# Kernel tuning notes

Measured on AMD Instinct MI355X. Metric: run time of the kernel, lower is better.

The kernel has to match this reference:

```python
import jax, jax.numpy as jnp
import numpy as np

B, C, H, W = 2, 256, 64, 64
HEADS, DIM_HEAD = 8, 64
INNER = HEADS * DIM_HEAD


def setup_inputs() -> dict:
    key = jax.random.key(0)
    k1, k2, k3, k4 = jax.random.split(key, 4)
    x = jax.random.normal(k1, (B, C, H, W), dtype=jnp.float32)
    # 1x1 conv weights stored as [out_ch, in_ch]
    w_qkv = jax.random.normal(k2, (3 * INNER, C), dtype=jnp.float32) * (1.0 / np.sqrt(C))
    w_out = jax.random.normal(k3, (C, INNER), dtype=jnp.float32) * (1.0 / np.sqrt(INNER))
    b_out = jax.random.normal(k4, (C,), dtype=jnp.float32) * 0.01
    return {"x": x, "w_qkv": w_qkv, "w_out": w_out, "b_out": b_out}


def reference(x, w_qkv, w_out, b_out):
    b, c, h, w = x.shape
    n = h * w
    # 1x1 conv == channel matmul
    qkv = jnp.einsum('oc,bchw->bohw', w_qkv, x)  # [B, 3*inner, H, W]
    qkv = qkv.reshape(b, 3, HEADS, DIM_HEAD, n)
    qkv = jnp.transpose(qkv, (1, 0, 2, 4, 3))    # [3, B, heads, N, dim_head]
    q, k, v = qkv[0], qkv[1], qkv[2]
    scale = 1.0 / (DIM_HEAD ** 0.5)
    dots = jnp.einsum('bhnd,bhmd->bhnm', q, k) * scale  # [B, heads, N, N]
    attn = jax.nn.softmax(dots, axis=-1)
    out = jnp.einsum('bhnm,bhmd->bhnd', attn, v)        # [B, heads, N, dim_head]
    out = jnp.transpose(out, (0, 1, 3, 2)).reshape(b, INNER, h, w)
    return jnp.einsum('ci,bihw->bchw', w_out, out) + b_out[None, :, None, None]
```

## Files before the change

kernel.cpp:

```cpp
#include <hip/hip_runtime.h>
#include <hip/hip_bf16.h>

typedef unsigned short u16;
typedef __attribute__((ext_vector_type(8))) short bf16x8;
typedef __attribute__((ext_vector_type(4))) float f32x4;
typedef __attribute__((ext_vector_type(8))) unsigned short u16x8;
typedef __attribute__((ext_vector_type(4))) unsigned short u16x4;

#define N_POS 4096
#define HEADS 8
#define DHEAD 64
#define CIN   256
#define INNER 512
#define NSPLIT 2
#define JCHUNK (N_POS / NSPLIT)

__device__ __forceinline__ u16 f2bf(float f) {
    union { float f; unsigned int u; } v; v.f = f;
    unsigned int u = v.u + 0x7FFFu + ((v.u >> 16) & 1u);
    return (u16)(u >> 16);
}

__device__ __forceinline__ float bf2f(u16 h) {
    union { float f; unsigned int u; } v; v.u = ((unsigned int)h) << 16;
    return v.f;
}

__device__ __forceinline__ unsigned int pkbf2(float lo, float hi) {
    union { __hip_bfloat162 b; unsigned int u; } cv;
    cv.b = __float22bfloat162_rn(make_float2(lo, hi));
    return cv.u;
}

__global__ __launch_bounds__(256, 2) void k1_qkv(const float* __restrict__ x,
                                                 const float* __restrict__ w_qkv,
                                                 const float* __restrict__ w_out,
                                                 u16* __restrict__ q_ws,
                                                 u16* __restrict__ k_ws,
                                                 u16* __restrict__ vt_ws,
                                                 u16* __restrict__ wo) {
    __shared__ u16 Alds[64 * 40];
    __shared__ u16 Blds[256 * 40];
    int tid = threadIdx.x;
    int by  = blockIdx.y;
    int b   = blockIdx.z;

    if (by == 24) {
        size_t base = ((size_t)((b * 16 + blockIdx.x) * 256 + tid)) * 16;
        const float* src = w_out + base;
        union { unsigned int u[4]; u16x8 v; } o0, o1;
        for (int j = 0; j < 4; ++j) o0.u[j] = pkbf2(src[2 * j],     src[2 * j + 1]);
        for (int j = 0; j < 4; ++j) o1.u[j] = pkbf2(src[8 + 2 * j], src[9 + 2 * j]);
        *(u16x8*)(wo + base)     = o0.v;
        *(u16x8*)(wo + base + 8) = o1.v;
        return;
    }

    int n0  = blockIdx.x * 256;
    int o0  = by * 64;
    int sel = by >> 3;
    int h   = by & 7;
    int wv = tid >> 6, l = tid & 63, quad = l >> 4, l15 = l & 15;
    int srow = tid >> 2, sseg = tid & 3;

    const float* xb = x + (size_t)b * CIN * N_POS + n0 + tid;

    f32x4 acc[16] = {};
    for (int c0 = 0; c0 < CIN; c0 += 32) {
        {
            const float* wqp = w_qkv + (size_t)(o0 + srow) * CIN + c0 + sseg * 8;
            union { unsigned int u[4]; u16x8 v; } av;
            for (int j = 0; j < 4; ++j) av.u[j] = pkbf2(wqp[2 * j], wqp[2 * j + 1]);
            *(u16x8*)&Alds[srow * 40 + sseg * 8] = av.v;
        }
        {
            union { unsigned int u[16]; } tmp;
            #pragma unroll
            for (int j = 0; j < 16; ++j)
                tmp.u[j] = pkbf2(xb[(size_t)(c0 + 2 * j) * N_POS],
                                 xb[(size_t)(c0 + 2 * j + 1) * N_POS]);
            u16* bd = &Blds[tid * 40];
            *(u16x8*)(bd)      = *(u16x8*)&tmp.u[0];
            *(u16x8*)(bd + 8)  = *(u16x8*)&tmp.u[4];
            *(u16x8*)(bd + 16) = *(u16x8*)&tmp.u[8];
            *(u16x8*)(bd + 24) = *(u16x8*)&tmp.u[12];
        }
        __syncthreads();
        bf16x8 af = *(const bf16x8*)&Alds[(wv * 16 + l15) * 40 + quad * 8];
        if (sel < 2) {
            for (int nt = 0; nt < 16; ++nt) {
                bf16x8 bfrag = *(const bf16x8*)&Blds[(nt * 16 + l15) * 40 + quad * 8];
                acc[nt] = __builtin_amdgcn_mfma_f32_16x16x32_bf16(af, bfrag, acc[nt], 0, 0, 0);
            }
        } else {
            for (int nt = 0; nt < 16; ++nt) {
                bf16x8 bfrag = *(const bf16x8*)&Blds[(nt * 16 + l15) * 40 + quad * 8];
                acc[nt] = __builtin_amdgcn_mfma_f32_16x16x32_bf16(bfrag, af, acc[nt], 0, 0, 0);
            }
        }
        __syncthreads();
    }
    const float QSCALE = 0.125f * 1.44269504088896f;
    int bh = b * HEADS + h;
    if (sel < 2) {
        float sc = (sel == 0) ? QSCALE : 1.0f;
        u16* base = (sel == 0) ? q_ws : k_ws;
        int dbase = wv * 16 + quad * 4;
        for (int nt = 0; nt < 16; ++nt) {
            int n = n0 + nt * 16 + l15;
            u16x4 pk;
            for (int r = 0; r < 4; ++r) pk[r] = f2bf(acc[nt][r] * sc);
            *(u16x4*)&base[((size_t)bh * N_POS + n) * DHEAD + dbase] = pk;
        }
    } else {
        int dloc = wv * 16 + l15;
        for (int nt = 0; nt < 16; ++nt) {
            u16x4 pk;
            for (int r = 0; r < 4; ++r) pk[r] = f2bf(acc[nt][r]);
            *(u16x4*)&vt_ws[((size_t)bh * DHEAD + dloc) * N_POS
                            + n0 + nt * 16 + quad * 4] = pk;
        }
    }
}

__global__ __launch_bounds__(256, 2) void k2_attn(const u16* __restrict__ q_ws,
                                                  const u16* __restrict__ k_ws,
                                                  const u16* __restrict__ vt_ws,
                                                  u16* __restrict__ op_ws,
                                                  float* __restrict__ lw_ws) {
    __shared__ u16 Klds[2][64 * 72];
    __shared__ u16 Vlds[2][80 * 72];
    int tid = threadIdx.x;
    int v   = blockIdx.x + (blockIdx.y << 4) + (blockIdx.z << 8);
    int slot = v & 7, idx = v >> 3;
    int bh   = slot * 2 + (idx & 1);
    int q0   = ((idx >> 1) & 15) * 256;
    int half = idx >> 5;
    int jbase = half * JCHUNK;
    int wv = tid >> 6, l = tid & 63, quad = l >> 4, l15 = l & 15;
    int srow = tid >> 2, sseg = tid & 3;
    int srowp = (srow & 0x23) | ((srow & 4) << 2) | ((srow & 0x18) >> 1);
    int kofs = srowp * 72 + sseg * 16;
    int vofs = srow * 72 + sseg * 16;

    const u16* qp = q_ws + ((size_t)(bh * N_POS + q0 + wv * 64 + l15)) * DHEAD + quad * 8;
    bf16x8 bq[4][2];
    for (int it = 0; it < 4; ++it) {
        bq[it][0] = *(const bf16x8*)(qp + (size_t)it * 16 * DHEAD);
        bq[it][1] = *(const bf16x8*)(qp + (size_t)it * 16 * DHEAD + 32);
    }

    f32x4 Oacc[4][5] = {};

    const u16* kp = k_ws + ((size_t)(bh * N_POS + srow)) * DHEAD + sseg * 16;
    const u16* vp = vt_ws + ((size_t)(bh * DHEAD + srow)) * N_POS + sseg * 16;

    {
        int r2 = tid >> 4, c4 = (tid & 15) * 4;
        u16 one = (r2 == 0) ? (u16)0x3F80 : (u16)0;
        u16x4 cv = {one, one, one, one};
        *(u16x4*)&Vlds[0][(64 + r2) * 72 + c4] = cv;
        *(u16x4*)&Vlds[1][(64 + r2) * 72 + c4] = cv;
    }

    u16x8 pf0 = *(const u16x8*)(kp + (size_t)jbase * DHEAD);
    u16x8 pf1 = *(const u16x8*)(kp + (size_t)jbase * DHEAD + 8);
    u16x8 pf2 = *(const u16x8*)(vp + jbase);
    u16x8 pf3 = *(const u16x8*)(vp + jbase + 8);
    *(u16x8*)&Klds[0][kofs]     = pf0;
    *(u16x8*)&Klds[0][kofs + 8] = pf1;
    *(u16x8*)&Vlds[0][vofs]     = pf2;
    *(u16x8*)&Vlds[0][vofs + 8] = pf3;
    {
        const u16* kpj = kp + (size_t)(jbase + 64) * DHEAD;
        pf0 = *(const u16x8*)kpj;
        pf1 = *(const u16x8*)(kpj + 8);
        pf2 = *(const u16x8*)(vp + jbase + 64);
        pf3 = *(const u16x8*)(vp + jbase + 72);
    }
    __syncthreads();

    union PF { unsigned int u[4]; bf16x8 v; };
    int cur = 0;
    for (int j0 = jbase; j0 < jbase + JCHUNK; j0 += 64) {
        if (j0 + 64 < jbase + JCHUNK) {
            *(u16x8*)&Klds[cur ^ 1][kofs]     = pf0;
            *(u16x8*)&Klds[cur ^ 1][kofs + 8] = pf1;
            *(u16x8*)&Vlds[cur ^ 1][vofs]     = pf2;
            *(u16x8*)&Vlds[cur ^ 1][vofs + 8] = pf3;
        }

        PF pfr[4][2];
        f32x4 z0[4], z1[4];

        auto QK = [&](f32x4* z, int p, int a) {
            const u16* kb = &Klds[cur][((2 * p + a) * 16 + l15) * 72 + quad * 8];
            bf16x8 kf0 = *(const bf16x8*)kb;
            bf16x8 kf1 = *(const bf16x8*)(kb + 32);
            __builtin_amdgcn_s_setprio(1);
            #pragma unroll
            for (int it = 0; it < 4; ++it) {
                f32x4 t = {};
                t = __builtin_amdgcn_mfma_f32_16x16x32_bf16(kf0, bq[it][0], t, 0, 0, 0);
                t = __builtin_amdgcn_mfma_f32_16x16x32_bf16(kf1, bq[it][1], t, 0, 0, 0);
                z[it] = t;
            }
            __builtin_amdgcn_s_setprio(0);
        };
        auto EXPPACK = [&](f32x4* z, int p, int a) {
            #pragma unroll
            for (int it = 0; it < 4; ++it) {
                float e0 = __builtin_amdgcn_exp2f(z[it][0]);
                float e1 = __builtin_amdgcn_exp2f(z[it][1]);
                float e2 = __builtin_amdgcn_exp2f(z[it][2]);
                float e3 = __builtin_amdgcn_exp2f(z[it][3]);
                pfr[it][p].u[2 * a]     = pkbf2(e0, e1);
                pfr[it][p].u[2 * a + 1] = pkbf2(e2, e3);
            }
        };
        auto PV = [&](int p, int dt_lo, int dt_hi) {
            __builtin_amdgcn_s_setprio(1);
            for (int dt = dt_lo; dt < dt_hi; ++dt) {
                bf16x8 vf = *(const bf16x8*)&Vlds[cur][(dt * 16 + l15) * 72 + p * 32 + quad * 8];
                #pragma unroll
                for (int it = 0; it < 4; ++it)
                    Oacc[it][dt] = __builtin_amdgcn_mfma_f32_16x16x32_bf16(vf, pfr[it][p].v, Oacc[it][dt], 0, 0, 0);
            }
            __builtin_amdgcn_s_setprio(0);
        };

        QK(z0, 0, 0);
        QK(z1, 0, 1);
        EXPPACK(z0, 0, 0);
        EXPPACK(z1, 0, 1);
        QK(z0, 1, 0);
        PV(0, 0, 2);
        EXPPACK(z0, 1, 0);
        QK(z1, 1, 1);
        PV(0, 2, 5);
        EXPPACK(z1, 1, 1);
        PV(1, 0, 5);

        if (j0 + 128 < jbase + JCHUNK) {
            const u16* kpj = kp + (size_t)(j0 + 128) * DHEAD;
            pf0 = *(const u16x8*)kpj;
            pf1 = *(const u16x8*)(kpj + 8);
            pf2 = *(const u16x8*)(vp + j0 + 128);
            pf3 = *(const u16x8*)(vp + j0 + 136);
        }
        __syncthreads();
        cur ^= 1;
    }

    int b = bh >> 3, h = bh & 7;
    u16* opb = op_ws + (size_t)half * 2 * N_POS * INNER;
    float* lwb = lw_ws + (size_t)half * 2 * HEADS * N_POS;
    for (int it = 0; it < 4; ++it) {
        int n = q0 + wv * 64 + it * 16 + l15;
        if (quad == 0) lwb[(size_t)bh * N_POS + n] = Oacc[it][4][0];
        u16* dst = opb + ((size_t)(b * N_POS + n)) * INNER + h * DHEAD;
        for (int dt = 0; dt < 4; ++dt) {
            u16x4 pk;
            for (int r = 0; r < 4; ++r) pk[r] = f2bf(Oacc[it][dt][r]);
            *(u16x4*)&dst[dt * 16 + quad * 4] = pk;
        }
    }
}

__global__ __launch_bounds__(512) void k3_out(const u16* __restrict__ wo,
                                              const float* __restrict__ b_out,
                                              const u16* __restrict__ op_ws,
                                              const float* __restrict__ lw_ws,
                                              float* __restrict__ out) {
    __shared__ u16 Alds[2][256 * 36];
    __shared__ u16 Blds[16 * 520];
    int tid = threadIdx.x;
    int n0 = blockIdx.x * 16;
    int b  = blockIdx.y;
    int wv = tid >> 6, l = tid & 63, quad = l >> 4, l15 = l & 15;

    {
        int i8 = tid & 63;
        int h  = i8 >> 3;
        for (int p = 0; p < 2; ++p) {
            int nl = p * 8 + (tid >> 6);
            int n = n0 + nl;
            size_t lidx = ((size_t)(b * HEADS + h)) * N_POS + n;
            float ls = lw_ws[lidx] + lw_ws[(size_t)2 * HEADS * N_POS + lidx];
            float inv = 1.0f / ls;
            size_t oidx = ((size_t)(b * N_POS + n)) * INNER + i8 * 8;
            u16x8 pv0 = *(const u16x8*)(op_ws + oidx);
            u16x8 pv1 = *(const u16x8*)(op_ws + (size_t)2 * N_POS * INNER + oidx);
            u16x8 vv;
            for (int k = 0; k < 8; ++k)
                vv[k] = f2bf((bf2f(pv0[k]) + bf2f(pv1[k])) * inv);
            *(u16x8*)&Blds[nl * 520 + i8 * 8] = vv;
        }
    }
    {
        int row = tid >> 1, seg = tid & 1;
        const u16* src = wo + (size_t)row * INNER + seg * 16;
        *(u16x8*)&Alds[0][row * 36 + seg * 16]     = *(const u16x8*)src;
        *(u16x8*)&Alds[0][row * 36 + seg * 16 + 8] = *(const u16x8*)(src + 8);
    }
    __syncthreads();

    f32x4 acc[2] = {};
    int cur = 0;
    for (int s = 0; s < 16; ++s) {
        if (s + 1 < 16) {
            int row = tid >> 1, seg = tid & 1;
            const u16* src = wo + (size_t)row * INNER + (s + 1) * 32 + seg * 16;
            *(u16x8*)&Alds[cur ^ 1][row * 36 + seg * 16]     = *(const u16x8*)src;
            *(u16x8*)&Alds[cur ^ 1][row * 36 + seg * 16 + 8] = *(const u16x8*)(src + 8);
        }
        for (int ac = 0; ac < 2; ++ac) {
            bf16x8 af = *(const bf16x8*)&Alds[cur][(wv * 32 + ac * 16 + l15) * 36 + quad * 8];
            bf16x8 bfrag = *(const bf16x8*)&Blds[l15 * 520 + s * 32 + quad * 8];
            acc[ac] = __builtin_amdgcn_mfma_f32_16x16x32_bf16(af, bfrag, acc[ac], 0, 0, 0);
        }
        __syncthreads();
        cur ^= 1;
    }
    for (int ac = 0; ac < 2; ++ac)
        for (int r = 0; r < 4; ++r) {
            int c = wv * 32 + ac * 16 + quad * 4 + r;
            out[((size_t)(b * CIN + c)) * N_POS + n0 + l15] = acc[ac][r] + b_out[c];
        }
}

extern "C" void kernel_launch(void* const* d_in, const int* in_sizes, int n_in,
                              void* d_out, int out_size, void* d_ws, size_t ws_size,
                              hipStream_t stream) {
    const float* x     = (const float*)d_in[0];
    const float* w_qkv = (const float*)d_in[1];
    const float* w_out = (const float*)d_in[2];
    const float* b_out = (const float*)d_in[3];
    float* out = (float*)d_out;

    u16* ws    = (u16*)d_ws;
    u16* q_ws  = ws;
    u16* k_ws  = q_ws + (size_t)2 * HEADS * N_POS * DHEAD;
    u16* vt_ws = k_ws + (size_t)2 * HEADS * N_POS * DHEAD;
    u16* wo_bf = vt_ws + (size_t)2 * HEADS * N_POS * DHEAD;
    u16* op_ws = wo_bf + (size_t)CIN * INNER;
    float* lw_ws = (float*)(op_ws + (size_t)NSPLIT * 2 * N_POS * INNER);

    hipLaunchKernelGGL(k1_qkv, dim3(16, 25, 2), dim3(256), 0, stream,
                       x, w_qkv, w_out, q_ws, k_ws, vt_ws, wo_bf);
    hipLaunchKernelGGL(k2_attn, dim3(16, 16, NSPLIT), dim3(256), 0, stream,
                       q_ws, k_ws, vt_ws, op_ws, lw_ws);
    hipLaunchKernelGGL(k3_out, dim3(256, 2), dim3(512), 0, stream,
                       wo_bf, b_out, op_ws, lw_ws, out);
}
```

Baseline: 175.1 us.

## Retile QKV projection so each block covers all heads for a 64-position slab

Result: slower. 196.7 us (+12.3%).

```diff
diff --git a/kernel.cpp b/kernel.cpp
--- a/kernel.cpp
+++ b/kernel.cpp
@@ -32,21 +32,22 @@
     return cv.u;
 }
 
-__global__ __launch_bounds__(256, 2) void k1_qkv(const float* __restrict__ x,
+__global__ __launch_bounds__(512, 2) void k1_qkv(const float* __restrict__ x,
                                                  const float* __restrict__ w_qkv,
                                                  const float* __restrict__ w_out,
                                                  u16* __restrict__ q_ws,
                                                  u16* __restrict__ k_ws,
                                                  u16* __restrict__ vt_ws,
                                                  u16* __restrict__ wo) {
-    __shared__ u16 Alds[64 * 40];
-    __shared__ u16 Blds[256 * 40];
+    __shared__ u16 Alds[512 * 40];
+    __shared__ u16 Blds[64 * 40];
     int tid = threadIdx.x;
     int by  = blockIdx.y;
     int b   = blockIdx.z;
 
-    if (by == 24) {
-        size_t base = ((size_t)((b * 16 + blockIdx.x) * 256 + tid)) * 16;
+    if (by == 3) {
+        if (blockIdx.x >= 8) return;
+        size_t base = ((size_t)((b * 8 + blockIdx.x) * 512 + tid)) * 16;
         const float* src = w_out + base;
         union { unsigned int u[4]; u16x8 v; } o0, o1;
         for (int j = 0; j < 4; ++j) o0.u[j] = pkbf2(src[2 * j],     src[2 * j + 1]);
@@ -56,69 +57,73 @@
         return;
     }
 
-    int n0  = blockIdx.x * 256;
-    int o0  = by * 64;
-    int sel = by >> 3;
-    int h   = by & 7;
+    int n0  = blockIdx.x * 64;
+    int sel = by;
     int wv = tid >> 6, l = tid & 63, quad = l >> 4, l15 = l & 15;
-    int srow = tid >> 2, sseg = tid & 3;
-
-    const float* xb = x + (size_t)b * CIN * N_POS + n0 + tid;
-
-    f32x4 acc[16] = {};
+
+    const float* xb = x + (size_t)b * CIN * N_POS + n0 + (tid & 63);
+    int xc = (tid >> 6) * 4;
+
+    f32x4 acc[4][4] = {};
     for (int c0 = 0; c0 < CIN; c0 += 32) {
         {
-            const float* wqp = w_qkv + (size_t)(o0 + srow) * CIN + c0 + sseg * 8;
-            union { unsigned int u[4]; u16x8 v; } av;
-            for (int j = 0; j < 4; ++j) av.u[j] = pkbf2(wqp[2 * j], wqp[2 * j + 1]);
-            *(u16x8*)&Alds[srow * 40 + sseg * 8] = av.v;
+            const float* wqp = w_qkv + (size_t)(sel * 512 + tid) * CIN + c0;
+            union { unsigned int u[4]; u16x8 v; } a0, a1, a2, a3;
+            for (int j = 0; j < 4; ++j) a0.u[j] = pkbf2(wqp[2 * j],      wqp[2 * j + 1]);
+            for (int j = 0; j < 4; ++j) a1.u[j] = pkbf2(wqp[8 + 2 * j],  wqp[9 + 2 * j]);
+            for (int j = 0; j < 4; ++j) a2.u[j] = pkbf2(wqp[16 + 2 * j], wqp[17 + 2 * j]);
+            for (int j = 0; j < 4; ++j) a3.u[j] = pkbf2(wqp[24 + 2 * j], wqp[25 + 2 * j]);
+            *(u16x8*)&Alds[tid * 40]      = a0.v;
+            *(u16x8*)&Alds[tid * 40 + 8]  = a1.v;
+            *(u16x8*)&Alds[tid * 40 + 16] = a2.v;
+            *(u16x8*)&Alds[tid * 40 + 24] = a3.v;
         }
         {
-            union { unsigned int u[16]; } tmp;
-            #pragma unroll
-            for (int j = 0; j < 16; ++j)
-                tmp.u[j] = pkbf2(xb[(size_t)(c0 + 2 * j) * N_POS],
-                                 xb[(size_t)(c0 + 2 * j + 1) * N_POS]);
-            u16* bd = &Blds[tid * 40];
-            *(u16x8*)(bd)      = *(u16x8*)&tmp.u[0];
-            *(u16x8*)(bd + 8)  = *(u16x8*)&tmp.u[4];
-            *(u16x8*)(bd + 16) = *(u16x8*)&tmp.u[8];
-            *(u16x8*)(bd + 24) = *(u16x8*)&tmp.u[12];
+            u16x4 bv;
+            for (int i = 0; i < 4; ++i)
+                bv[i] = f2bf(xb[(size_t)(c0 + xc + i) * N_POS]);
+            *(u16x4*)&Blds[(tid & 63) * 40 + xc] = bv;
         }
         __syncthreads();
-        bf16x8 af = *(const bf16x8*)&Alds[(wv * 16 + l15) * 40 + quad * 8];
-        if (sel < 2) {
-            for (int nt = 0; nt < 16; ++nt) {
-                bf16x8 bfrag = *(const bf16x8*)&Blds[(nt * 16 + l15) * 40 + quad * 8];
-                acc[nt] = __builtin_amdgcn_mfma_f32_16x16x32_bf16(af, bfrag, acc[nt], 0, 0, 0);
-            }
-        } else {
-            for (int nt = 0; nt < 16; ++nt) {
-                bf16x8 bfrag = *(const bf16x8*)&Blds[(nt * 16 + l15) * 40 + quad * 8];
-                acc[nt] = __builtin_amdgcn_mfma_f32_16x16x32_bf16(bfrag, af, acc[nt], 0, 0, 0);
+        for (int ot = 0; ot < 4; ++ot) {
+            bf16x8 af = *(const bf16x8*)&Alds[(wv * 64 + ot * 16 + l15) * 40 + quad * 8];
+            if (sel < 2) {
+                for (int nt = 0; nt < 4; ++nt) {
+                    bf16x8 bfrag = *(const bf16x8*)&Blds[(nt * 16 + l15) * 40 + quad * 8];
+                    acc[ot][nt] = __builtin_amdgcn_mfma_f32_16x16x32_bf16(af, bfrag, acc[ot][nt], 0, 0, 0);
+                }
+            } else {
+                for (int nt = 0; nt < 4; ++nt) {
+                    bf16x8 bfrag = *(const bf16x8*)&Blds[(nt * 16 + l15) * 40 + quad * 8];
+                    acc[ot][nt] = __builtin_amdgcn_mfma_f32_16x16x32_bf16(bfrag, af, acc[ot][nt], 0, 0, 0);
+                }
             }
         }
         __syncthreads();
     }
     const float QSCALE = 0.125f * 1.44269504088896f;
-    int bh = b * HEADS + h;
+    int bh = b * HEADS + wv;
     if (sel < 2) {
         float sc = (sel == 0) ? QSCALE : 1.0f;
         u16* base = (sel == 0) ? q_ws : k_ws;
-        int dbase = wv * 16 + quad * 4;
-        for (int nt = 0; nt < 16; ++nt) {
-            int n = n0 + nt * 16 + l15;
-            u16x4 pk;
-            for (int r = 0; r < 4; ++r) pk[r] = f2bf(acc[nt][r] * sc);
-            *(u16x4*)&base[((size_t)bh * N_POS + n) * DHEAD + dbase] = pk;
+        for (int ot = 0; ot < 4; ++ot) {
+            int dbase = ot * 16 + quad * 4;
+            for (int nt = 0; nt < 4; ++nt) {
+                int n = n0 + nt * 16 + l15;
+                u16x4 pk;
+                for (int r = 0; r < 4; ++r) pk[r] = f2bf(acc[ot][nt][r] * sc);
+                *(u16x4*)&base[((size_t)bh * N_POS + n) * DHEAD + dbase] = pk;
+            }
         }
     } else {
-        int dloc = wv * 16 + l15;
-        for (int nt = 0; nt < 16; ++nt) {
-            u16x4 pk;
-            for (int r = 0; r < 4; ++r) pk[r] = f2bf(acc[nt][r]);
-            *(u16x4*)&vt_ws[((size_t)bh * DHEAD + dloc) * N_POS
-                            + n0 + nt * 16 + quad * 4] = pk;
+        for (int ot = 0; ot < 4; ++ot) {
+            int dloc = ot * 16 + l15;
+            for (int nt = 0; nt < 4; ++nt) {
+                u16x4 pk;
+                for (int r = 0; r < 4; ++r) pk[r] = f2bf(acc[ot][nt][r]);
+                *(u16x4*)&vt_ws[((size_t)bh * DHEAD + dloc) * N_POS
+                                + n0 + nt * 16 + quad * 4] = pk;
+            }
         }
     }
 }
@@ -346,7 +351,7 @@
     u16* op_ws = wo_bf + (size_t)CIN * INNER;
     float* lw_ws = (float*)(op_ws + (size_t)NSPLIT * 2 * N_POS * INNER);
 
-    hipLaunchKernelGGL(k1_qkv, dim3(16, 25, 2), dim3(256), 0, stream,
+    hipLaunchKernelGGL(k1_qkv, dim3(64, 4, 2), dim3(512), 0, stream,
                        x, w_qkv, w_out, q_ws, k_ws, vt_ws, wo_bf);
     hipLaunchKernelGGL(k2_attn, dim3(16, 16, NSPLIT), dim3(256), 0, stream,
                        q_ws, k_ws, vt_ws, op_ws, lw_ws);
```
